# Kernel optimization log

Hardware: AMD Instinct MI355X
Metric: run time of the kernel (lower is better)

Reference implementation:

```python
import jax, jax.numpy as jnp
import numpy as np
import math

T, B, I, N, O = 512, 256, 128, 1024, 10
H_STEP = 0.1
ALPHA = 1.0
OMEGA = 1.0
GAMMA = 0.1
OMEGA_FACTOR = OMEGA * OMEGA
GAMMA_FACTOR = 2.0 * GAMMA
GAIN_REC = 1.0 / math.sqrt(N)


def setup_inputs() -> dict:
    key = jax.random.key(0)
    ks = jax.random.split(key, 7)
    # torch.nn.Linear default init: U(-1/sqrt(fan_in), 1/sqrt(fan_in))
    def lin(kw, kb, fan_out, fan_in):
        bound = 1.0 / math.sqrt(fan_in)
        w = jax.random.uniform(kw, (fan_out, fan_in), minval=-bound, maxval=bound, dtype=jnp.float32)
        b = jax.random.uniform(kb, (fan_out,), minval=-bound, maxval=bound, dtype=jnp.float32)
        return w, b
    i2h_w, i2h_b = lin(ks[0], ks[1], N, I)
    h2h_w, h2h_b = lin(ks[2], ks[3], N, N)
    h2o_w, h2o_b = lin(ks[4], ks[5], O, N)
    batch = jax.random.normal(ks[6], (T, B, I), dtype=jnp.float32)
    return {
        "batch": batch,
        "i2h_w": i2h_w, "i2h_b": i2h_b,
        "h2h_w": h2h_w, "h2h_b": h2h_b,
        "h2o_w": h2o_w, "h2o_b": h2o_b,
    }


def reference(batch, i2h_w, i2h_b, h2h_w, h2h_b, h2o_w, h2o_b):
    # Precompute input projection for all timesteps: [T, B, N]
    inp_proj = jnp.einsum('tbi,ni->tbn', batch, i2h_w) + i2h_b

    def step(carry, u_t):
        x_t, y_t = carry  # each [B, N]
        rec = GAIN_REC * (y_t @ h2h_w.T + h2h_b)  # gain scales full h2h(y) incl. bias
        y_t = y_t + H_STEP * (ALPHA * jnp.tanh(u_t + rec)
                              - OMEGA_FACTOR * x_t - GAMMA_FACTOR * y_t)
        x_t = x_t + H_STEP * y_t
        return (x_t, y_t), None

    x0 = jnp.zeros((batch.shape[1], h2h_w.shape[0]), dtype=batch.dtype)
    y0 = jnp.zeros_like(x0)
    (x_T, _), _ = jax.lax.scan(step, (x0, y0), inp_proj)
    output = x_T @ h2o_w.T + h2o_b  # [B, O]
    return output
```

## Files before the change

### kernel.cpp

```cpp
#include <hip/hip_runtime.h>

#define T_STEPS 512
#define BATCH_N 256
#define IDIM    128
#define NDIM    1024
#define ODIM    10

#define THREADS 256
#define GAIN 0.03125f

#define YBUF_OFF    (33554432ull)
#define YBUF_HALF   (524288ull)
#define YHALF_EL    (262144u)
#define FLG_OFF     (YBUF_OFF + 2*YBUF_HALF)
#define FLG_BYTES   (2048ull)
#define XT_OFF      (FLG_OFF + FLG_BYTES)
#define XT_BYTES    (1048576ull)
#define WS_NEED     (XT_OFF + XT_BYTES)

typedef short    s16x8 __attribute__((ext_vector_type(8)));
typedef float    f32x4 __attribute__((ext_vector_type(4)));
typedef unsigned u32x4 __attribute__((ext_vector_type(4)));

__device__ __forceinline__ unsigned short f2bf(float f) {
  unsigned u = __builtin_bit_cast(unsigned, f);
  u += 0x7fffu + ((u >> 16) & 1u);
  return (unsigned short)(u >> 16);
}

__global__ void horn_convert(const float* __restrict__ src, unsigned short* __restrict__ dst) {
  size_t gid = (size_t)blockIdx.x * 256 + threadIdx.x;
  const f32x4* s4 = reinterpret_cast<const f32x4*>(src) + gid * 2;
  f32x4 a = s4[0], b = s4[1];
  u32x4 o;
  o[0] = (unsigned)f2bf(a[0]) | ((unsigned)f2bf(a[1]) << 16);
  o[1] = (unsigned)f2bf(a[2]) | ((unsigned)f2bf(a[3]) << 16);
  o[2] = (unsigned)f2bf(b[0]) | ((unsigned)f2bf(b[1]) << 16);
  o[3] = (unsigned)f2bf(b[2]) | ((unsigned)f2bf(b[3]) << 16);
  reinterpret_cast<u32x4*>(dst)[gid] = o;
}

__launch_bounds__(THREADS, 1)
__global__ void horn_persistent(const unsigned short* __restrict__ batchbf,
                                const float* __restrict__ i2h_w,
                                const float* __restrict__ i2h_b,
                                const float* __restrict__ h2h_w,
                                const float* __restrict__ h2h_b,
                                unsigned short* ybuf,
                                unsigned int*  flags,
                                float* xT)
{
  __shared__ char  ylds[32768];
  __shared__ f32x4 red[4][4][64];

  const int tid  = threadIdx.x;
  const int lane = tid & 63;
  const int wv   = tid >> 6;
  const int blk  = blockIdx.x;
  const int ig   = blk & 15;
  const int jg   = blk >> 4;
  const int l15  = lane & 15;
  const int kb   = lane >> 4;
  const int jc   = jg * 64 + wv * 16 + l15;

  s16x8 wfrag[4][8];
  #pragma unroll
  for (int ct = 0; ct < 4; ++ct) {
    #pragma unroll
    for (int kc = 0; kc < 8; ++kc) {
      const float* gp = h2h_w + (size_t)(jg * 64 + ct * 16 + l15) * NDIM
                        + wv * 256 + kc * 32 + kb * 8;
      f32x4 a = *reinterpret_cast<const f32x4*>(gp);
      f32x4 b = *reinterpret_cast<const f32x4*>(gp + 4);
      s16x8 v;
      v[0] = (short)f2bf(a[0]*GAIN); v[1] = (short)f2bf(a[1]*GAIN);
      v[2] = (short)f2bf(a[2]*GAIN); v[3] = (short)f2bf(a[3]*GAIN);
      v[4] = (short)f2bf(b[0]*GAIN); v[5] = (short)f2bf(b[1]*GAIN);
      v[6] = (short)f2bf(b[2]*GAIN); v[7] = (short)f2bf(b[3]*GAIN);
      wfrag[ct][kc] = v;
    }
  }

  s16x8 i2hf[4];
  #pragma unroll
  for (int kc = 0; kc < 4; ++kc) {
    const float* gp = i2h_w + (size_t)jc * IDIM + kc * 32 + kb * 8;
    s16x8 v;
    #pragma unroll
    for (int e = 0; e < 8; ++e) v[e] = (short)f2bf(gp[e]);
    i2hf[kc] = v;
  }
  const float bias = i2h_b[jc] + GAIN * h2h_b[jc];

  s16x8 bfr[4];
  {
    const unsigned short* bp = batchbf + ((size_t)ig * 16 + l15) * IDIM + kb * 8;
    #pragma unroll
    for (int kc = 0; kc < 4; ++kc) bfr[kc] = *reinterpret_cast<const s16x8*>(bp + kc * 32);
  }

  float xs[4] = {0.f,0.f,0.f,0.f};
  float ys[4] = {0.f,0.f,0.f,0.f};

  const char* ytile = (const char*)ybuf + (size_t)ig * 32768;
  unsigned short* pub0 = ybuf + (size_t)(ig * 16 + kb * 4) * 1024 + jc;
  const unsigned* fline = flags + ig * 32 + l15;
  unsigned* fstore = flags + ig * 32 + jg;

  for (int t = 0; t < T_STEPS; ++t) {
    const int p = t & 1, pn = p ^ 1;

    if (t > 0) {
      if (wv == 0) {
        while (true) {
          unsigned fv;
          asm volatile("global_load_dword %0, %1, off sc0 sc1\n\t"
                       "s_waitcnt vmcnt(0)"
                       : "=v"(fv) : "v"(fline) : "memory");
          if (__all((int)fv >= t)) break;
          __builtin_amdgcn_s_sleep(1);
        }
      }
      __syncthreads();
    }

    const char* q0 = ytile + (size_t)p * YBUF_HALF + tid * 16;
    u32x4 v0, v1, v2, v3, v4, v5, v6, v7;
    asm volatile(
      "global_load_dwordx4 %0, %8, off sc0 sc1\n\t"
      "global_load_dwordx4 %1, %9, off sc0 sc1\n\t"
      "global_load_dwordx4 %2, %10, off sc0 sc1\n\t"
      "global_load_dwordx4 %3, %11, off sc0 sc1\n\t"
      "global_load_dwordx4 %4, %12, off sc0 sc1\n\t"
      "global_load_dwordx4 %5, %13, off sc0 sc1\n\t"
      "global_load_dwordx4 %6, %14, off sc0 sc1\n\t"
      "global_load_dwordx4 %7, %15, off sc0 sc1"
      : "=&v"(v0), "=&v"(v1), "=&v"(v2), "=&v"(v3),
        "=&v"(v4), "=&v"(v5), "=&v"(v6), "=&v"(v7)
      : "v"(q0), "v"(q0 + 4096), "v"(q0 + 8192), "v"(q0 + 12288),
        "v"(q0 + 16384), "v"(q0 + 20480), "v"(q0 + 24576), "v"(q0 + 28672)
      : "memory");

    f32x4 uacc = {bias, bias, bias, bias};
    #pragma unroll
    for (int kc = 0; kc < 4; ++kc)
      uacc = __builtin_amdgcn_mfma_f32_16x16x32_bf16(bfr[kc], i2hf[kc], uacc, 0, 0, 0);

    asm volatile("s_waitcnt vmcnt(0)" ::: "memory");
    __builtin_amdgcn_sched_barrier(0);

    #define STG(r, vr) { int B_ = (r) * 4096 + tid * 16; int row_ = B_ >> 11; \
      *reinterpret_cast<u32x4*>(ylds + (B_ ^ ((row_ & 7) << 4))) = vr; }
    STG(0, v0) STG(1, v1) STG(2, v2) STG(3, v3)
    STG(4, v4) STG(5, v5) STG(6, v6) STG(7, v7)
    #undef STG
    __syncthreads();

    f32x4 c0 = {0,0,0,0}, c1 = {0,0,0,0}, c2 = {0,0,0,0}, c3 = {0,0,0,0};
    #pragma unroll
    for (int kc = 0; kc < 8; ++kc) {
      int boff = (l15 * 2048 + wv * 512 + kc * 64 + kb * 16) ^ ((l15 & 7) << 4);
      s16x8 a = *reinterpret_cast<const s16x8*>(ylds + boff);
      c0 = __builtin_amdgcn_mfma_f32_16x16x32_bf16(a, wfrag[0][kc], c0, 0, 0, 0);
      c1 = __builtin_amdgcn_mfma_f32_16x16x32_bf16(a, wfrag[1][kc], c1, 0, 0, 0);
      c2 = __builtin_amdgcn_mfma_f32_16x16x32_bf16(a, wfrag[2][kc], c2, 0, 0, 0);
      c3 = __builtin_amdgcn_mfma_f32_16x16x32_bf16(a, wfrag[3][kc], c3, 0, 0, 0);
    }

    red[wv][0][lane] = c0;
    red[wv][1][lane] = c1;
    red[wv][2][lane] = c2;
    red[wv][3][lane] = c3;
    __syncthreads();
    f32x4 z = uacc;
    z += red[0][wv][lane];
    z += red[1][wv][lane];
    z += red[2][wv][lane];
    z += red[3][wv][lane];

    unsigned yw0, yw1, yw2, yw3;
    {
      float zz, e, r, th, yn;
      zz = z[0]; e = __expf(zz + zz); r = __builtin_amdgcn_rcpf(e + 1.0f); th = fmaf(-2.0f, r, 1.0f);
      yn = ys[0] + 0.1f*(th - xs[0] - 0.2f*ys[0]); xs[0] += 0.1f*yn; ys[0] = yn; yw0 = f2bf(yn);
      zz = z[1]; e = __expf(zz + zz); r = __builtin_amdgcn_rcpf(e + 1.0f); th = fmaf(-2.0f, r, 1.0f);
      yn = ys[1] + 0.1f*(th - xs[1] - 0.2f*ys[1]); xs[1] += 0.1f*yn; ys[1] = yn; yw1 = f2bf(yn);
      zz = z[2]; e = __expf(zz + zz); r = __builtin_amdgcn_rcpf(e + 1.0f); th = fmaf(-2.0f, r, 1.0f);
      yn = ys[2] + 0.1f*(th - xs[2] - 0.2f*ys[2]); xs[2] += 0.1f*yn; ys[2] = yn; yw2 = f2bf(yn);
      zz = z[3]; e = __expf(zz + zz); r = __builtin_amdgcn_rcpf(e + 1.0f); th = fmaf(-2.0f, r, 1.0f);
      yn = ys[3] + 0.1f*(th - xs[3] - 0.2f*ys[3]); xs[3] += 0.1f*yn; ys[3] = yn; yw3 = f2bf(yn);
    }

    {
      unsigned short* b0 = pub0 + (size_t)pn * YHALF_EL;
      unsigned short* b1 = b0 + 2 * NDIM;
      asm volatile(
        "global_store_short %4, %0, off offset:0    sc0 sc1\n\t"
        "global_store_short %4, %1, off offset:2048 sc0 sc1\n\t"
        "global_store_short %5, %2, off offset:0    sc0 sc1\n\t"
        "global_store_short %5, %3, off offset:2048 sc0 sc1"
        :
        : "v"(yw0), "v"(yw1), "v"(yw2), "v"(yw3), "v"(b0), "v"(b1)
        : "memory");
    }
    {
      const int tn = (t + 1 < T_STEPS) ? (t + 1) : t;
      const unsigned short* bp = batchbf + ((size_t)tn * BATCH_N + ig * 16 + l15) * IDIM + kb * 8;
      #pragma unroll
      for (int kc = 0; kc < 4; ++kc) bfr[kc] = *reinterpret_cast<const s16x8*>(bp + kc * 32);
    }
    asm volatile("s_waitcnt vmcnt(0)" ::: "memory");
    __syncthreads();
    if (tid == 0) {
      unsigned nv = (unsigned)(t + 1);
      asm volatile("global_store_dword %0, %1, off sc0 sc1"
                   :: "v"(fstore), "v"(nv) : "memory");
    }
  }

  #pragma unroll
  for (int q = 0; q < 4; ++q) {
    int row = ig * 16 + kb * 4 + q;
    xT[(size_t)row * NDIM + jc] = xs[q];
  }
}

__global__ void horn_out(const float* __restrict__ xT, const float* __restrict__ h2o_w,
                         const float* __restrict__ h2o_b, float* __restrict__ out) {
  int b = blockIdx.x;
  int lane = threadIdx.x;
  float p[ODIM];
  #pragma unroll
  for (int o = 0; o < ODIM; ++o) p[o] = 0.f;
  for (int it = 0; it < NDIM / 64; ++it) {
    int n = it * 64 + lane;
    float xv = xT[(size_t)b * NDIM + n];
    #pragma unroll
    for (int o = 0; o < ODIM; ++o) p[o] += xv * h2o_w[o * NDIM + n];
  }
  #pragma unroll
  for (int o = 0; o < ODIM; ++o) {
    float v = p[o];
    #pragma unroll
    for (int off = 32; off >= 1; off >>= 1) v += __shfl_down(v, off, 64);
    if (lane == 0) out[b * ODIM + o] = v + h2o_b[o];
  }
}

__global__ void horn_fail(float* out) {
  int i = blockIdx.x * 256 + threadIdx.x;
  if (i < BATCH_N * ODIM) out[i] = 12345.0f;
}

extern "C" void kernel_launch(void* const* d_in, const int* in_sizes, int n_in,
                              void* d_out, int out_size, void* d_ws, size_t ws_size,
                              hipStream_t stream) {
  const float* batch = (const float*)d_in[0];
  const float* i2h_w = (const float*)d_in[1];
  const float* i2h_b = (const float*)d_in[2];
  const float* h2h_w = (const float*)d_in[3];
  const float* h2h_b = (const float*)d_in[4];
  const float* h2o_w = (const float*)d_in[5];
  const float* h2o_b = (const float*)d_in[6];
  float* out = (float*)d_out;
  char* ws = (char*)d_ws;

  if (ws_size < WS_NEED) {
    horn_fail<<<16, 256, 0, stream>>>(out);
    return;
  }

  hipMemsetAsync(ws + YBUF_OFF, 0, YBUF_HALF, stream);
  hipMemsetAsync(ws + FLG_OFF, 0, FLG_BYTES, stream);

  horn_convert<<<8192, 256, 0, stream>>>(batch, (unsigned short*)(ws + 0));

  horn_persistent<<<256, THREADS, 0, stream>>>(
      (const unsigned short*)(ws + 0), i2h_w, i2h_b, h2h_w, h2h_b,
      (unsigned short*)(ws + YBUF_OFF), (unsigned int*)(ws + FLG_OFF),
      (float*)(ws + XT_OFF));

  horn_out<<<BATCH_N, 64, 0, stream>>>((const float*)(ws + XT_OFF), h2o_w, h2o_b, out);
}
```

Baseline: 1.522 ms.

## Interleave two batch groups per block to overlap sync latency with compute

Each persistent block now owns two batch row-groups instead of one, halving the grid to 128 blocks. It alternates between them so that while one group's recurrent matmul and update run, the other group's y tile and input batch are being loaded. Flags become per-wave and are published earlier, and the batch input is staged through LDS together with the y tile in a single load bundle. The intent is to hide the inter-block flag-wait and global-load latency on the serial recurrence, at the cost of half as many CUs doing work and more complex ordering that is easy to get wrong.

```diff
diff --git a/kernel.cpp b/kernel.cpp
--- a/kernel.cpp
+++ b/kernel.cpp
@@ -13,7 +13,7 @@
 #define YBUF_HALF   (524288ull)
 #define YHALF_EL    (262144u)
 #define FLG_OFF     (YBUF_OFF + 2*YBUF_HALF)
-#define FLG_BYTES   (2048ull)
+#define FLG_BYTES   (8192ull)
 #define XT_OFF      (FLG_OFF + FLG_BYTES)
 #define XT_BYTES    (1048576ull)
 #define WS_NEED     (XT_OFF + XT_BYTES)
@@ -52,23 +52,24 @@
 {
   __shared__ char  ylds[32768];
   __shared__ f32x4 red[4][4][64];
+  __shared__ char  batchL[2][4096];
 
   const int tid  = threadIdx.x;
   const int lane = tid & 63;
   const int wv   = tid >> 6;
-  const int blk  = blockIdx.x;
-  const int ig   = blk & 15;
-  const int jg   = blk >> 4;
+  const int pr   = blockIdx.x & 7;
+  const int s    = blockIdx.x >> 3;
   const int l15  = lane & 15;
   const int kb   = lane >> 4;
-  const int jc   = jg * 64 + wv * 16 + l15;
+  const int jc   = s * 64 + wv * 16 + l15;
+  const int gidx[2] = {pr, pr + 8};
 
   s16x8 wfrag[4][8];
   #pragma unroll
   for (int ct = 0; ct < 4; ++ct) {
     #pragma unroll
     for (int kc = 0; kc < 8; ++kc) {
-      const float* gp = h2h_w + (size_t)(jg * 64 + ct * 16 + l15) * NDIM
+      const float* gp = h2h_w + (size_t)(s * 64 + ct * 16 + l15) * NDIM
                         + wv * 256 + kc * 32 + kb * 8;
       f32x4 a = *reinterpret_cast<const f32x4*>(gp);
       f32x4 b = *reinterpret_cast<const f32x4*>(gp + 4);
@@ -80,7 +81,6 @@
       wfrag[ct][kc] = v;
     }
   }
-
   s16x8 i2hf[4];
   #pragma unroll
   for (int kc = 0; kc < 4; ++kc) {
@@ -92,136 +92,156 @@
   }
   const float bias = i2h_b[jc] + GAIN * h2h_b[jc];
 
-  s16x8 bfr[4];
+  const char* gb[2];
+  unsigned short* pub0[2];
+  const unsigned* flp[2];
+  unsigned* fs[2];
+  #pragma unroll
+  for (int X = 0; X < 2; ++X) {
+    int g = gidx[X];
+    gb[X]   = (const char*)ybuf + (size_t)g * 32768 + (size_t)tid * 16;
+    pub0[X] = ybuf + (size_t)(g * 16 + kb * 4) * 1024 + jc;
+    flp[X]  = flags + g * 64 + lane;
+    fs[X]   = flags + g * 64 + s * 4 + wv;
+  }
+  unsigned* dmy = flags + 1024 + blockIdx.x * 8 + wv;
+  const char* bbase = (const char*)batchbf;
+  const int batch_lane = tid * 16;
+  const int brow = tid >> 4, bcp = tid & 15;
+  const int bldsoff = brow * 256 + ((bcp ^ (brow & 7)) << 4);
+
+  float xs[2][4] = {{0,0,0,0},{0,0,0,0}};
+  float ys[2][4] = {{0,0,0,0},{0,0,0,0}};
+
+  u32x4 vy0, vy1, vy2, vy3, vy4, vy5, vy6, vy7, vbat;
+
+  #define GBUNDLE(YB, BP)                                                   \
+    { const char* y_ = (YB);                                                \
+      asm volatile(                                                         \
+        "global_load_dwordx4 %0, %9, off sc0 sc1\n\t"                       \
+        "global_load_dwordx4 %1, %10, off sc0 sc1\n\t"                      \
+        "global_load_dwordx4 %2, %11, off sc0 sc1\n\t"                      \
+        "global_load_dwordx4 %3, %12, off sc0 sc1\n\t"                      \
+        "global_load_dwordx4 %4, %13, off sc0 sc1\n\t"                      \
+        "global_load_dwordx4 %5, %14, off sc0 sc1\n\t"                      \
+        "global_load_dwordx4 %6, %15, off sc0 sc1\n\t"                      \
+        "global_load_dwordx4 %7, %16, off sc0 sc1\n\t"                      \
+        "global_load_dwordx4 %8, %17, off"                                  \
+        : "=&v"(vy0), "=&v"(vy1), "=&v"(vy2), "=&v"(vy3),                   \
+          "=&v"(vy4), "=&v"(vy5), "=&v"(vy6), "=&v"(vy7), "=&v"(vbat)       \
+        : "v"(y_), "v"(y_+4096), "v"(y_+8192), "v"(y_+12288),               \
+          "v"(y_+16384), "v"(y_+20480), "v"(y_+24576), "v"(y_+28672),       \
+          "v"(BP)                                                           \
+        : "memory"); }
+
+  #define STG(r, vr) { int B_ = (r) * 4096 + tid * 16; int row_ = B_ >> 11; \
+    *reinterpret_cast<u32x4*>(ylds + (B_ ^ ((row_ & 7) << 4))) = vr; }
+
+  #define UPD(X, r, yw) { float z_ = z[r];                                  \
+    float e_ = __expf(z_ + z_);                                             \
+    float th_ = fmaf(-2.0f, __builtin_amdgcn_rcpf(e_ + 1.0f), 1.0f);        \
+    float yn_ = ys[X][r] + 0.1f*(th_ - xs[X][r] - 0.2f*ys[X][r]);           \
+    xs[X][r] += 0.1f*yn_; ys[X][r] = yn_; yw = f2bf(yn_); }
+
+  #define SERVICE(X, OX, TFLAG, TSPIN, TISS, DOISS, PN)                     \
+  {                                                                         \
+    asm volatile("s_waitcnt vmcnt(4)" ::: "memory");                        \
+    __builtin_amdgcn_sched_barrier(0);                                      \
+    STG(0, vy0) STG(1, vy1) STG(2, vy2) STG(3, vy3)                         \
+    STG(4, vy4) STG(5, vy5) STG(6, vy6) STG(7, vy7)                         \
+    *reinterpret_cast<u32x4*>(&batchL[X][bldsoff]) = vbat;                  \
+    asm volatile("s_waitcnt vmcnt(0)" ::: "memory");                        \
+    __builtin_amdgcn_sched_barrier(0);                                      \
+    __syncthreads();                          \
+    if (lane == 0) {                                                        \
+      unsigned fv_ = (unsigned)(TFLAG);                                     \
+      asm volatile("global_store_dword %0, %1, off sc0 sc1"                 \
+                   :: "v"(fs[OX]), "v"(fv_) : "memory");                    \
+    }                                                                       \
+    f32x4 uacc = {bias, bias, bias, bias};                                  \
+    _Pragma("unroll")                                                       \
+    for (int kc = 0; kc < 4; ++kc) {                                        \
+      s16x8 a_ = *reinterpret_cast<const s16x8*>(                           \
+          &batchL[X][l15 * 256 + (((kc * 4 + kb) ^ (l15 & 7)) << 4)]);      \
+      uacc = __builtin_amdgcn_mfma_f32_16x16x32_bf16(a_, i2hf[kc], uacc, 0, 0, 0); \
+    }                                                                       \
+    f32x4 c0 = {0,0,0,0}, c1 = {0,0,0,0}, c2 = {0,0,0,0}, c3 = {0,0,0,0};   \
+    _Pragma("unroll")                                                       \
+    for (int kc = 0; kc < 8; ++kc) {                                        \
+      int boff = (l15 * 2048 + wv * 512 + kc * 64 + kb * 16) ^ ((l15 & 7) << 4); \
+      s16x8 a_ = *reinterpret_cast<const s16x8*>(ylds + boff);              \
+      c0 = __builtin_amdgcn_mfma_f32_16x16x32_bf16(a_, wfrag[0][kc], c0, 0, 0, 0); \
+      c1 = __builtin_amdgcn_mfma_f32_16x16x32_bf16(a_, wfrag[1][kc], c1, 0, 0, 0); \
+      c2 = __builtin_amdgcn_mfma_f32_16x16x32_bf16(a_, wfrag[2][kc], c2, 0, 0, 0); \
+      c3 = __builtin_amdgcn_mfma_f32_16x16x32_bf16(a_, wfrag[3][kc], c3, 0, 0, 0); \
+    }                                                                       \
+    red[wv][0][lane] = c0; red[wv][1][lane] = c1;                           \
+    red[wv][2][lane] = c2; red[wv][3][lane] = c3;                           \
+    if (DOISS) {                                                            \
+      while (true) { unsigned pv_;                                          \
+        asm volatile("global_load_dword %0, %1, off sc0 sc1\n\t"            \
+                     "s_waitcnt vmcnt(0)"                                   \
+                     : "=v"(pv_) : "v"(flp[OX]) : "memory");                \
+        if (__all((int)pv_ >= (TSPIN))) break;                              \
+        __builtin_amdgcn_s_sleep(1);                                        \
+      }                                                                     \
+      const char* ya_ = gb[OX] + (size_t)((TISS) & 1) * YBUF_HALF;          \
+      const char* ba_ = bbase + ((size_t)(TISS) * 256 + gidx[OX] * 16) * 256 + batch_lane; \
+      GBUNDLE(ya_, ba_)                                                     \
+    }                                                                       \
+    asm volatile("s_waitcnt lgkmcnt(0)" ::: "memory");                      \
+    __builtin_amdgcn_sched_barrier(0);                                      \
+    __builtin_amdgcn_s_barrier();           \
+    __builtin_amdgcn_sched_barrier(0);                                      \
+    f32x4 z = uacc;                                                         \
+    z += red[0][wv][lane]; z += red[1][wv][lane];                           \
+    z += red[2][wv][lane]; z += red[3][wv][lane];                           \
+    unsigned yw0, yw1, yw2, yw3;                                            \
+    UPD(X, 0, yw0) UPD(X, 1, yw1) UPD(X, 2, yw2) UPD(X, 3, yw3)             \
+    { unsigned short* b0 = pub0[X] + (size_t)(PN) * YHALF_EL;               \
+      unsigned short* b1 = b0 + 2 * NDIM;                                   \
+      asm volatile(                                                         \
+        "global_store_short %4, %0, off offset:0    sc0 sc1\n\t"            \
+        "global_store_short %4, %1, off offset:2048 sc0 sc1\n\t"            \
+        "global_store_short %5, %2, off offset:0    sc0 sc1\n\t"            \
+        "global_store_short %5, %3, off offset:2048 sc0 sc1"                \
+        :: "v"(yw0), "v"(yw1), "v"(yw2), "v"(yw3), "v"(b0), "v"(b1)         \
+        : "memory"); }                                                      \
+  }
+
+  asm volatile("s_waitcnt vmcnt(0)" ::: "memory");
   {
-    const unsigned short* bp = batchbf + ((size_t)ig * 16 + l15) * IDIM + kb * 8;
-    #pragma unroll
-    for (int kc = 0; kc < 4; ++kc) bfr[kc] = *reinterpret_cast<const s16x8*>(bp + kc * 32);
-  }
-
-  float xs[4] = {0.f,0.f,0.f,0.f};
-  float ys[4] = {0.f,0.f,0.f,0.f};
-
-  const char* ytile = (const char*)ybuf + (size_t)ig * 32768;
-  unsigned short* pub0 = ybuf + (size_t)(ig * 16 + kb * 4) * 1024 + jc;
-  const unsigned* fline = flags + ig * 32 + l15;
-  unsigned* fstore = flags + ig * 32 + jg;
-
+    const char* ya_ = gb[0];
+    const char* ba_ = bbase + ((size_t)gidx[0] * 16) * 256 + batch_lane;
+    GBUNDLE(ya_, ba_)
+    unsigned z0 = 0u;
+    asm volatile(
+      "global_store_dword %0, %1, off sc0 sc1\n\t"
+      "global_store_dword %0, %1, off sc0 sc1\n\t"
+      "global_store_dword %0, %1, off sc0 sc1\n\t"
+      "global_store_dword %0, %1, off sc0 sc1"
+      :: "v"(dmy), "v"(z0) : "memory");
+  }
+
+  #pragma unroll 1
   for (int t = 0; t < T_STEPS; ++t) {
     const int p = t & 1, pn = p ^ 1;
-
-    if (t > 0) {
-      if (wv == 0) {
-        while (true) {
-          unsigned fv;
-          asm volatile("global_load_dword %0, %1, off sc0 sc1\n\t"
-                       "s_waitcnt vmcnt(0)"
-                       : "=v"(fv) : "v"(fline) : "memory");
-          if (__all((int)fv >= t)) break;
-          __builtin_amdgcn_s_sleep(1);
-        }
-      }
-      __syncthreads();
-    }
-
-    const char* q0 = ytile + (size_t)p * YBUF_HALF + tid * 16;
-    u32x4 v0, v1, v2, v3, v4, v5, v6, v7;
-    asm volatile(
-      "global_load_dwordx4 %0, %8, off sc0 sc1\n\t"
-      "global_load_dwordx4 %1, %9, off sc0 sc1\n\t"
-      "global_load_dwordx4 %2, %10, off sc0 sc1\n\t"
-      "global_load_dwordx4 %3, %11, off sc0 sc1\n\t"
-      "global_load_dwordx4 %4, %12, off sc0 sc1\n\t"
-      "global_load_dwordx4 %5, %13, off sc0 sc1\n\t"
-      "global_load_dwordx4 %6, %14, off sc0 sc1\n\t"
-      "global_load_dwordx4 %7, %15, off sc0 sc1"
-      : "=&v"(v0), "=&v"(v1), "=&v"(v2), "=&v"(v3),
-        "=&v"(v4), "=&v"(v5), "=&v"(v6), "=&v"(v7)
-      : "v"(q0), "v"(q0 + 4096), "v"(q0 + 8192), "v"(q0 + 12288),
-        "v"(q0 + 16384), "v"(q0 + 20480), "v"(q0 + 24576), "v"(q0 + 28672)
-      : "memory");
-
-    f32x4 uacc = {bias, bias, bias, bias};
-    #pragma unroll
-    for (int kc = 0; kc < 4; ++kc)
-      uacc = __builtin_amdgcn_mfma_f32_16x16x32_bf16(bfr[kc], i2hf[kc], uacc, 0, 0, 0);
-
-    asm volatile("s_waitcnt vmcnt(0)" ::: "memory");
-    __builtin_amdgcn_sched_barrier(0);
-
-    #define STG(r, vr) { int B_ = (r) * 4096 + tid * 16; int row_ = B_ >> 11; \
-      *reinterpret_cast<u32x4*>(ylds + (B_ ^ ((row_ & 7) << 4))) = vr; }
-    STG(0, v0) STG(1, v1) STG(2, v2) STG(3, v3)
-    STG(4, v4) STG(5, v5) STG(6, v6) STG(7, v7)
-    #undef STG
-    __syncthreads();
-
-    f32x4 c0 = {0,0,0,0}, c1 = {0,0,0,0}, c2 = {0,0,0,0}, c3 = {0,0,0,0};
-    #pragma unroll
-    for (int kc = 0; kc < 8; ++kc) {
-      int boff = (l15 * 2048 + wv * 512 + kc * 64 + kb * 16) ^ ((l15 & 7) << 4);
-      s16x8 a = *reinterpret_cast<const s16x8*>(ylds + boff);
-      c0 = __builtin_amdgcn_mfma_f32_16x16x32_bf16(a, wfrag[0][kc], c0, 0, 0, 0);
-      c1 = __builtin_amdgcn_mfma_f32_16x16x32_bf16(a, wfrag[1][kc], c1, 0, 0, 0);
-      c2 = __builtin_amdgcn_mfma_f32_16x16x32_bf16(a, wfrag[2][kc], c2, 0, 0, 0);
-      c3 = __builtin_amdgcn_mfma_f32_16x16x32_bf16(a, wfrag[3][kc], c3, 0, 0, 0);
-    }
-
-    red[wv][0][lane] = c0;
-    red[wv][1][lane] = c1;
-    red[wv][2][lane] = c2;
-    red[wv][3][lane] = c3;
-    __syncthreads();
-    f32x4 z = uacc;
-    z += red[0][wv][lane];
-    z += red[1][wv][lane];
-    z += red[2][wv][lane];
-    z += red[3][wv][lane];
-
-    unsigned yw0, yw1, yw2, yw3;
-    {
-      float zz, e, r, th, yn;
-      zz = z[0]; e = __expf(zz + zz); r = __builtin_amdgcn_rcpf(e + 1.0f); th = fmaf(-2.0f, r, 1.0f);
-      yn = ys[0] + 0.1f*(th - xs[0] - 0.2f*ys[0]); xs[0] += 0.1f*yn; ys[0] = yn; yw0 = f2bf(yn);
-      zz = z[1]; e = __expf(zz + zz); r = __builtin_amdgcn_rcpf(e + 1.0f); th = fmaf(-2.0f, r, 1.0f);
-      yn = ys[1] + 0.1f*(th - xs[1] - 0.2f*ys[1]); xs[1] += 0.1f*yn; ys[1] = yn; yw1 = f2bf(yn);
-      zz = z[2]; e = __expf(zz + zz); r = __builtin_amdgcn_rcpf(e + 1.0f); th = fmaf(-2.0f, r, 1.0f);
-      yn = ys[2] + 0.1f*(th - xs[2] - 0.2f*ys[2]); xs[2] += 0.1f*yn; ys[2] = yn; yw2 = f2bf(yn);
-      zz = z[3]; e = __expf(zz + zz); r = __builtin_amdgcn_rcpf(e + 1.0f); th = fmaf(-2.0f, r, 1.0f);
-      yn = ys[3] + 0.1f*(th - xs[3] - 0.2f*ys[3]); xs[3] += 0.1f*yn; ys[3] = yn; yw3 = f2bf(yn);
-    }
-
-    {
-      unsigned short* b0 = pub0 + (size_t)pn * YHALF_EL;
-      unsigned short* b1 = b0 + 2 * NDIM;
-      asm volatile(
-        "global_store_short %4, %0, off offset:0    sc0 sc1\n\t"
-        "global_store_short %4, %1, off offset:2048 sc0 sc1\n\t"
-        "global_store_short %5, %2, off offset:0    sc0 sc1\n\t"
-        "global_store_short %5, %3, off offset:2048 sc0 sc1"
-        :
-        : "v"(yw0), "v"(yw1), "v"(yw2), "v"(yw3), "v"(b0), "v"(b1)
-        : "memory");
-    }
-    {
-      const int tn = (t + 1 < T_STEPS) ? (t + 1) : t;
-      const unsigned short* bp = batchbf + ((size_t)tn * BATCH_N + ig * 16 + l15) * IDIM + kb * 8;
-      #pragma unroll
-      for (int kc = 0; kc < 4; ++kc) bfr[kc] = *reinterpret_cast<const s16x8*>(bp + kc * 32);
-    }
-    asm volatile("s_waitcnt vmcnt(0)" ::: "memory");
-    __syncthreads();
-    if (tid == 0) {
-      unsigned nv = (unsigned)(t + 1);
-      asm volatile("global_store_dword %0, %1, off sc0 sc1"
-                   :: "v"(fstore), "v"(nv) : "memory");
-    }
-  }
+    SERVICE(0, 1, t, t, t, 1, pn)
+    SERVICE(1, 0, t + 1, t + 1, t + 1, (t < T_STEPS - 1), pn)
+  }
+  #undef SERVICE
+  #undef GBUNDLE
+  #undef STG
+  #undef UPD
+
+  asm volatile("s_waitcnt vmcnt(0)" ::: "memory");
 
   #pragma unroll
   for (int q = 0; q < 4; ++q) {
-    int row = ig * 16 + kb * 4 + q;
-    xT[(size_t)row * NDIM + jc] = xs[q];
+    int rowA = gidx[0] * 16 + kb * 4 + q;
+    int rowB = gidx[1] * 16 + kb * 4 + q;
+    xT[(size_t)rowA * NDIM + jc] = xs[0][q];
+    xT[(size_t)rowB * NDIM + jc] = xs[1][q];
   }
 }
 
@@ -275,7 +295,7 @@
 
   horn_convert<<<8192, 256, 0, stream>>>(batch, (unsigned short*)(ws + 0));
 
-  horn_persistent<<<256, THREADS, 0, stream>>>(
+  horn_persistent<<<128, THREADS, 0, stream>>>(
       (const unsigned short*)(ws + 0), i2h_w, i2h_b, h2h_w, h2h_b,
       (unsigned short*)(ws + YBUF_OFF), (unsigned int*)(ws + FLG_OFF),
       (float*)(ws + XT_OFF));
```

Measured after the change: 2.175 ms. 42.9% more time.

## Use per-wave flags and wave-private LDS staging to drop block barriers

Applied to the files above, without the earlier changes.

Each wave now polls and sets its own flag (64 flags per batch group) and stages only the y slice it consumes into a private LDS region, so two of the three per-step __syncthreads are removed. The reduction buffer is double-buffered by step parity so one barrier per step suffices. Step 0 is peeled, which skips the zero y matmul and the ybuf memset. The batch prefetch uses inline asm issued after the flag store. The aim is to shorten the serial per-step critical path, at the cost of more flag traffic and polling lanes.

```diff
diff --git a/kernel.cpp b/kernel.cpp
--- a/kernel.cpp
+++ b/kernel.cpp
@@ -13,7 +13,7 @@
 #define YBUF_HALF   (524288ull)
 #define YHALF_EL    (262144u)
 #define FLG_OFF     (YBUF_OFF + 2*YBUF_HALF)
-#define FLG_BYTES   (2048ull)
+#define FLG_BYTES   (4096ull)
 #define XT_OFF      (FLG_OFF + FLG_BYTES)
 #define XT_BYTES    (1048576ull)
 #define WS_NEED     (XT_OFF + XT_BYTES)
@@ -51,7 +51,7 @@
                                 float* xT)
 {
   __shared__ char  ylds[32768];
-  __shared__ f32x4 red[4][4][64];
+  __shared__ f32x4 red[2][16][64];
 
   const int tid  = threadIdx.x;
   const int lane = tid & 63;
@@ -80,7 +80,6 @@
       wfrag[ct][kc] = v;
     }
   }
-
   s16x8 i2hf[4];
   #pragma unroll
   for (int kc = 0; kc < 4; ++kc) {
@@ -92,131 +91,158 @@
   }
   const float bias = i2h_b[jc] + GAIN * h2h_b[jc];
 
-  s16x8 bfr[4];
+  const char* gb0 = (const char*)ybuf + (size_t)ig * 32768
+                    + (size_t)(lane >> 5) * 2048 + wv * 512 + (lane & 31) * 16;
+  unsigned short* pub0 = ybuf + (size_t)(ig * 16 + kb * 4) * 1024 + jc;
+  const unsigned* fpoll = flags + ig * 64 + lane;
+  unsigned* fstore = flags + ig * 64 + jg * 4 + wv;
+  const char* bb = (const char*)batchbf;
+  const size_t boff_lane = (size_t)(ig * 16 + l15) * 256 + kb * 16;
+
+  float xs[4] = {0,0,0,0}, ys[4] = {0,0,0,0};
+  u32x4 pf0, pf1, pf2, pf3;
+  u32x4 gy0, gy1, gy2, gy3, gy4, gy5, gy6, gy7;
+
+  #define PREFETCH(T) { const char* bp_ = bb + (size_t)(T) * 65536 + boff_lane; \
+    asm volatile( \
+      "global_load_dwordx4 %0, %4, off offset:0\n\t"  \
+      "global_load_dwordx4 %1, %4, off offset:64\n\t" \
+      "global_load_dwordx4 %2, %4, off offset:128\n\t"\
+      "global_load_dwordx4 %3, %4, off offset:192"    \
+      : "=&v"(pf0), "=&v"(pf1), "=&v"(pf2), "=&v"(pf3) : "v"(bp_) : "memory"); }
+
+  #define UPHASE(uacc) { \
+    uacc = __builtin_amdgcn_mfma_f32_16x16x32_bf16(__builtin_bit_cast(s16x8, pf0), i2hf[0], uacc, 0, 0, 0); \
+    uacc = __builtin_amdgcn_mfma_f32_16x16x32_bf16(__builtin_bit_cast(s16x8, pf1), i2hf[1], uacc, 0, 0, 0); \
+    uacc = __builtin_amdgcn_mfma_f32_16x16x32_bf16(__builtin_bit_cast(s16x8, pf2), i2hf[2], uacc, 0, 0, 0); \
+    uacc = __builtin_amdgcn_mfma_f32_16x16x32_bf16(__builtin_bit_cast(s16x8, pf3), i2hf[3], uacc, 0, 0, 0); }
+
+  #define UPD4(z) \
+    unsigned yw0, yw1, yw2, yw3; { float z_, e_, th_, yn_; \
+    z_ = z[0]; e_ = __expf(z_ + z_); th_ = fmaf(-2.0f, __builtin_amdgcn_rcpf(e_ + 1.0f), 1.0f); \
+    yn_ = ys[0] + 0.1f*(th_ - xs[0] - 0.2f*ys[0]); xs[0] += 0.1f*yn_; ys[0] = yn_; yw0 = f2bf(yn_); \
+    z_ = z[1]; e_ = __expf(z_ + z_); th_ = fmaf(-2.0f, __builtin_amdgcn_rcpf(e_ + 1.0f), 1.0f); \
+    yn_ = ys[1] + 0.1f*(th_ - xs[1] - 0.2f*ys[1]); xs[1] += 0.1f*yn_; ys[1] = yn_; yw1 = f2bf(yn_); \
+    z_ = z[2]; e_ = __expf(z_ + z_); th_ = fmaf(-2.0f, __builtin_amdgcn_rcpf(e_ + 1.0f), 1.0f); \
+    yn_ = ys[2] + 0.1f*(th_ - xs[2] - 0.2f*ys[2]); xs[2] += 0.1f*yn_; ys[2] = yn_; yw2 = f2bf(yn_); \
+    z_ = z[3]; e_ = __expf(z_ + z_); th_ = fmaf(-2.0f, __builtin_amdgcn_rcpf(e_ + 1.0f), 1.0f); \
+    yn_ = ys[3] + 0.1f*(th_ - xs[3] - 0.2f*ys[3]); xs[3] += 0.1f*yn_; ys[3] = yn_; yw3 = f2bf(yn_); }
+
+  #define PUBLISH(PN) { \
+    unsigned short* b0_ = pub0 + (size_t)(PN) * YHALF_EL; \
+    unsigned short* b1_ = b0_ + 2 * NDIM; \
+    asm volatile( \
+      "global_store_short %4, %0, off offset:0    sc0 sc1\n\t" \
+      "global_store_short %4, %1, off offset:2048 sc0 sc1\n\t" \
+      "global_store_short %5, %2, off offset:0    sc0 sc1\n\t" \
+      "global_store_short %5, %3, off offset:2048 sc0 sc1" \
+      :: "v"(yw0), "v"(yw1), "v"(yw2), "v"(yw3), "v"(b0_), "v"(b1_) : "memory"); }
+
+  #define SETFLAG(V) { unsigned nv_ = (unsigned)(V); \
+    asm volatile("global_store_dword %0, %1, off sc0 sc1" :: "v"(fstore), "v"(nv_) : "memory"); }
+
+  PREFETCH(0)
+  asm volatile("s_waitcnt vmcnt(0)" ::: "memory");
+  __builtin_amdgcn_sched_barrier(0);
   {
-    const unsigned short* bp = batchbf + ((size_t)ig * 16 + l15) * IDIM + kb * 8;
-    #pragma unroll
-    for (int kc = 0; kc < 4; ++kc) bfr[kc] = *reinterpret_cast<const s16x8*>(bp + kc * 32);
-  }
-
-  float xs[4] = {0.f,0.f,0.f,0.f};
-  float ys[4] = {0.f,0.f,0.f,0.f};
-
-  const char* ytile = (const char*)ybuf + (size_t)ig * 32768;
-  unsigned short* pub0 = ybuf + (size_t)(ig * 16 + kb * 4) * 1024 + jc;
-  const unsigned* fline = flags + ig * 32 + l15;
-  unsigned* fstore = flags + ig * 32 + jg;
-
-  for (int t = 0; t < T_STEPS; ++t) {
+    f32x4 uacc = {bias, bias, bias, bias};
+    UPHASE(uacc)
+    UPD4(uacc)
+    PUBLISH(1)
+    asm volatile("s_waitcnt vmcnt(0)" ::: "memory");
+    SETFLAG(1)
+    PREFETCH(1)
+  }
+
+  #pragma unroll 1
+  for (int t = 1; t < T_STEPS; ++t) {
     const int p = t & 1, pn = p ^ 1;
 
-    if (t > 0) {
-      if (wv == 0) {
-        while (true) {
-          unsigned fv;
-          asm volatile("global_load_dword %0, %1, off sc0 sc1\n\t"
-                       "s_waitcnt vmcnt(0)"
-                       : "=v"(fv) : "v"(fline) : "memory");
-          if (__all((int)fv >= t)) break;
-          __builtin_amdgcn_s_sleep(1);
-        }
-      }
-      __syncthreads();
-    }
-
-    const char* q0 = ytile + (size_t)p * YBUF_HALF + tid * 16;
-    u32x4 v0, v1, v2, v3, v4, v5, v6, v7;
-    asm volatile(
-      "global_load_dwordx4 %0, %8, off sc0 sc1\n\t"
-      "global_load_dwordx4 %1, %9, off sc0 sc1\n\t"
-      "global_load_dwordx4 %2, %10, off sc0 sc1\n\t"
-      "global_load_dwordx4 %3, %11, off sc0 sc1\n\t"
-      "global_load_dwordx4 %4, %12, off sc0 sc1\n\t"
-      "global_load_dwordx4 %5, %13, off sc0 sc1\n\t"
-      "global_load_dwordx4 %6, %14, off sc0 sc1\n\t"
-      "global_load_dwordx4 %7, %15, off sc0 sc1"
-      : "=&v"(v0), "=&v"(v1), "=&v"(v2), "=&v"(v3),
-        "=&v"(v4), "=&v"(v5), "=&v"(v6), "=&v"(v7)
-      : "v"(q0), "v"(q0 + 4096), "v"(q0 + 8192), "v"(q0 + 12288),
-        "v"(q0 + 16384), "v"(q0 + 20480), "v"(q0 + 24576), "v"(q0 + 28672)
-      : "memory");
+    while (true) {
+      unsigned fv;
+      asm volatile("global_load_dword %0, %1, off sc0 sc1\n\ts_waitcnt vmcnt(0)"
+                   : "=v"(fv) : "v"(fpoll) : "memory");
+      if (__all((int)fv >= t)) break;
+      __builtin_amdgcn_s_sleep(1);
+    }
+    __builtin_amdgcn_sched_barrier(0);
+
+    {
+      const char* g0 = gb0 + (size_t)p * YBUF_HALF;
+      asm volatile(
+        "global_load_dwordx4 %0, %8, off sc0 sc1\n\t"
+        "global_load_dwordx4 %1, %9, off sc0 sc1\n\t"
+        "global_load_dwordx4 %2, %10, off sc0 sc1\n\t"
+        "global_load_dwordx4 %3, %11, off sc0 sc1\n\t"
+        "global_load_dwordx4 %4, %12, off sc0 sc1\n\t"
+        "global_load_dwordx4 %5, %13, off sc0 sc1\n\t"
+        "global_load_dwordx4 %6, %14, off sc0 sc1\n\t"
+        "global_load_dwordx4 %7, %15, off sc0 sc1"
+        : "=&v"(gy0), "=&v"(gy1), "=&v"(gy2), "=&v"(gy3),
+          "=&v"(gy4), "=&v"(gy5), "=&v"(gy6), "=&v"(gy7)
+        : "v"(g0), "v"(g0 + 4096), "v"(g0 + 8192), "v"(g0 + 12288),
+          "v"(g0 + 16384), "v"(g0 + 20480), "v"(g0 + 24576), "v"(g0 + 28672)
+        : "memory");
+    }
 
     f32x4 uacc = {bias, bias, bias, bias};
-    #pragma unroll
-    for (int kc = 0; kc < 4; ++kc)
-      uacc = __builtin_amdgcn_mfma_f32_16x16x32_bf16(bfr[kc], i2hf[kc], uacc, 0, 0, 0);
+    UPHASE(uacc)
 
     asm volatile("s_waitcnt vmcnt(0)" ::: "memory");
     __builtin_amdgcn_sched_barrier(0);
 
-    #define STG(r, vr) { int B_ = (r) * 4096 + tid * 16; int row_ = B_ >> 11; \
-      *reinterpret_cast<u32x4*>(ylds + (B_ ^ ((row_ & 7) << 4))) = vr; }
-    STG(0, v0) STG(1, v1) STG(2, v2) STG(3, v3)
-    STG(4, v4) STG(5, v5) STG(6, v6) STG(7, v7)
-    #undef STG
-    __syncthreads();
+    {
+      char* base = ylds + wv * 8192;
+      int h = lane >> 5, c16 = (lane & 31) << 4;
+      #define STG(i, vr) { int row_ = 2 * (i) + h; \
+        *reinterpret_cast<u32x4*>(base + row_ * 512 + (c16 ^ ((row_ & 7) << 4))) = vr; }
+      STG(0, gy0) STG(1, gy1) STG(2, gy2) STG(3, gy3)
+      STG(4, gy4) STG(5, gy5) STG(6, gy6) STG(7, gy7)
+      #undef STG
+    }
+    asm volatile("s_waitcnt lgkmcnt(0)" ::: "memory");
+    __builtin_amdgcn_sched_barrier(0);
 
     f32x4 c0 = {0,0,0,0}, c1 = {0,0,0,0}, c2 = {0,0,0,0}, c3 = {0,0,0,0};
-    #pragma unroll
-    for (int kc = 0; kc < 8; ++kc) {
-      int boff = (l15 * 2048 + wv * 512 + kc * 64 + kb * 16) ^ ((l15 & 7) << 4);
-      s16x8 a = *reinterpret_cast<const s16x8*>(ylds + boff);
-      c0 = __builtin_amdgcn_mfma_f32_16x16x32_bf16(a, wfrag[0][kc], c0, 0, 0, 0);
-      c1 = __builtin_amdgcn_mfma_f32_16x16x32_bf16(a, wfrag[1][kc], c1, 0, 0, 0);
-      c2 = __builtin_amdgcn_mfma_f32_16x16x32_bf16(a, wfrag[2][kc], c2, 0, 0, 0);
-      c3 = __builtin_amdgcn_mfma_f32_16x16x32_bf16(a, wfrag[3][kc], c3, 0, 0, 0);
-    }
-
-    red[wv][0][lane] = c0;
-    red[wv][1][lane] = c1;
-    red[wv][2][lane] = c2;
-    red[wv][3][lane] = c3;
+    {
+      const char* base = ylds + wv * 8192 + l15 * 512;
+      const int swz = (l15 & 7) << 4;
+      #pragma unroll
+      for (int kc = 0; kc < 8; ++kc) {
+        s16x8 a = *reinterpret_cast<const s16x8*>(base + ((kc * 64 + kb * 16) ^ swz));
+        c0 = __builtin_amdgcn_mfma_f32_16x16x32_bf16(a, wfrag[0][kc], c0, 0, 0, 0);
+        c1 = __builtin_amdgcn_mfma_f32_16x16x32_bf16(a, wfrag[1][kc], c1, 0, 0, 0);
+        c2 = __builtin_amdgcn_mfma_f32_16x16x32_bf16(a, wfrag[2][kc], c2, 0, 0, 0);
+        c3 = __builtin_amdgcn_mfma_f32_16x16x32_bf16(a, wfrag[3][kc], c3, 0, 0, 0);
+      }
+    }
+
+    red[p][wv * 4 + 0][lane] = c0;
+    red[p][wv * 4 + 1][lane] = c1;
+    red[p][wv * 4 + 2][lane] = c2;
+    red[p][wv * 4 + 3][lane] = c3;
     __syncthreads();
     f32x4 z = uacc;
-    z += red[0][wv][lane];
-    z += red[1][wv][lane];
-    z += red[2][wv][lane];
-    z += red[3][wv][lane];
-
-    unsigned yw0, yw1, yw2, yw3;
-    {
-      float zz, e, r, th, yn;
-      zz = z[0]; e = __expf(zz + zz); r = __builtin_amdgcn_rcpf(e + 1.0f); th = fmaf(-2.0f, r, 1.0f);
-      yn = ys[0] + 0.1f*(th - xs[0] - 0.2f*ys[0]); xs[0] += 0.1f*yn; ys[0] = yn; yw0 = f2bf(yn);
-      zz = z[1]; e = __expf(zz + zz); r = __builtin_amdgcn_rcpf(e + 1.0f); th = fmaf(-2.0f, r, 1.0f);
-      yn = ys[1] + 0.1f*(th - xs[1] - 0.2f*ys[1]); xs[1] += 0.1f*yn; ys[1] = yn; yw1 = f2bf(yn);
-      zz = z[2]; e = __expf(zz + zz); r = __builtin_amdgcn_rcpf(e + 1.0f); th = fmaf(-2.0f, r, 1.0f);
-      yn = ys[2] + 0.1f*(th - xs[2] - 0.2f*ys[2]); xs[2] += 0.1f*yn; ys[2] = yn; yw2 = f2bf(yn);
-      zz = z[3]; e = __expf(zz + zz); r = __builtin_amdgcn_rcpf(e + 1.0f); th = fmaf(-2.0f, r, 1.0f);
-      yn = ys[3] + 0.1f*(th - xs[3] - 0.2f*ys[3]); xs[3] += 0.1f*yn; ys[3] = yn; yw3 = f2bf(yn);
-    }
-
-    {
-      unsigned short* b0 = pub0 + (size_t)pn * YHALF_EL;
-      unsigned short* b1 = b0 + 2 * NDIM;
-      asm volatile(
-        "global_store_short %4, %0, off offset:0    sc0 sc1\n\t"
-        "global_store_short %4, %1, off offset:2048 sc0 sc1\n\t"
-        "global_store_short %5, %2, off offset:0    sc0 sc1\n\t"
-        "global_store_short %5, %3, off offset:2048 sc0 sc1"
-        :
-        : "v"(yw0), "v"(yw1), "v"(yw2), "v"(yw3), "v"(b0), "v"(b1)
-        : "memory");
-    }
-    {
-      const int tn = (t + 1 < T_STEPS) ? (t + 1) : t;
-      const unsigned short* bp = batchbf + ((size_t)tn * BATCH_N + ig * 16 + l15) * IDIM + kb * 8;
-      #pragma unroll
-      for (int kc = 0; kc < 4; ++kc) bfr[kc] = *reinterpret_cast<const s16x8*>(bp + kc * 32);
-    }
+    z += red[p][0 * 4 + wv][lane];
+    z += red[p][1 * 4 + wv][lane];
+    z += red[p][2 * 4 + wv][lane];
+    z += red[p][3 * 4 + wv][lane];
+
+    UPD4(z)
+    PUBLISH(pn)
     asm volatile("s_waitcnt vmcnt(0)" ::: "memory");
-    __syncthreads();
-    if (tid == 0) {
-      unsigned nv = (unsigned)(t + 1);
-      asm volatile("global_store_dword %0, %1, off sc0 sc1"
-                   :: "v"(fstore), "v"(nv) : "memory");
-    }
-  }
+    SETFLAG(t + 1)
+    const int tn = (t + 1 < T_STEPS) ? (t + 1) : t;
+    PREFETCH(tn)
+  }
+
+  #undef PREFETCH
+  #undef UPHASE
+  #undef UPD4
+  #undef PUBLISH
+  #undef SETFLAG
+
+  asm volatile("s_waitcnt vmcnt(0)" ::: "memory");
 
   #pragma unroll
   for (int q = 0; q < 4; ++q) {
@@ -270,7 +296,6 @@
     return;
   }
 
-  hipMemsetAsync(ws + YBUF_OFF, 0, YBUF_HALF, stream);
   hipMemsetAsync(ws + FLG_OFF, 0, FLG_BYTES, stream);
 
   horn_convert<<<8192, 256, 0, stream>>>(batch, (unsigned short*)(ws + 0));
```

Result: slower. 4.644 ms (+205.1%).
